# Performance work log

Measured on AMD Instinct MI355X. Metric: run time of the kernel, lower is better.

## Reference

```python
import jax, jax.numpy as jnp
import numpy as np

C = 512      # filters
G = 32       # groups
EPS = 1e-6

def setup_inputs() -> dict:
    key = jax.random.key(0)
    ks = jax.random.split(key, 10)
    B, H, W = 2, 64, 64
    inputs = jax.random.normal(ks[0], (B, H, W, C), dtype=jnp.float32)
    scale = 1.0 / np.sqrt(C)
    def w(k):
        return jax.random.normal(k, (C, C), dtype=jnp.float32) * scale
    return {
        "inputs": inputs,
        "gn_gamma": jnp.ones((C,), jnp.float32),
        "gn_beta": jnp.zeros((C,), jnp.float32),
        "wq": w(ks[1]), "bq": jnp.zeros((C,), jnp.float32),
        "wk": w(ks[2]), "bk": jnp.zeros((C,), jnp.float32),
        "wv": w(ks[3]), "bv": jnp.zeros((C,), jnp.float32),
        "wo": w(ks[4]), "bo": jnp.zeros((C,), jnp.float32),
    }

def _group_norm(x, gamma, beta):
    B, H, W, c = x.shape
    xg = x.reshape(B, H, W, G, c // G)
    mean = jnp.mean(xg, axis=(1, 2, 4), keepdims=True)
    var = jnp.var(xg, axis=(1, 2, 4), keepdims=True)
    xg = (xg - mean) * jax.lax.rsqrt(var + EPS)
    return xg.reshape(B, H, W, c) * gamma + beta

def reference(inputs, gn_gamma, gn_beta, wq, bq, wk, bk, wv, bv, wo, bo):
    B, H, W, c = inputs.shape
    x = _group_norm(inputs, gn_gamma, gn_beta)
    # 1x1 convs == per-pixel linear layers
    q = (x @ wq + bq).reshape(B, H * W, c)
    k = (x @ wk + bk).reshape(B, H * W, c)
    v = (x @ wv + bv).reshape(B, H * W, c)
    q = q * jnp.asarray(1.0 / np.sqrt(float(c)), q.dtype)
    scores = jnp.einsum('bnc,bmc->bnm', q, k).astype(jnp.float32)  # [B,N,N]
    probs = jax.nn.softmax(scores, axis=-1).astype(inputs.dtype)
    attn = jnp.einsum('bnm,bmc->bnc', probs, v)
    out = attn.reshape(B, H, W, c) @ wo + bo
    return out + inputs
```

## Files before the change

### kernel.cpp

```cpp
#include <hip/hip_runtime.h>
#include <math.h>

typedef __bf16 bf16;
typedef __bf16 bf16x8 __attribute__((ext_vector_type(8)));
typedef float  f32x4  __attribute__((ext_vector_type(4)));

#define DEV __device__ __forceinline__

DEV void gload_lds16(const bf16* g, bf16* l) {
  __builtin_amdgcn_global_load_lds(
      (const __attribute__((address_space(1))) void*)g,
      (__attribute__((address_space(3))) void*)l, 16, 0, 0);
}

#define OFF_STATS 0UL
#define OFF_XN    512UL
#define OFF_WTQKV 8389120UL
#define OFF_WOT   9961984UL
#define OFF_BIASQ 10486272UL
#define OFF_QKV   10492416UL
#define OFF_VT    35658240UL
#define OFF_S     44046848UL
#define OFF_ATTN  111155712UL

__global__ __launch_bounds__(256) void gn_part_k(const float* __restrict__ x,
                                                 float2* __restrict__ part) {
  const int blk = blockIdx.x;
  const int chunk = blk & 15;
  const int bg = blk >> 4;
  const int b = bg >> 5, g = bg & 31;
  const int t = threadIdx.x;
  const int p = chunk * 256 + t;
  const float* xp = x + (size_t)b * (4096 * 512) + (size_t)p * 512 + g * 16;
  float4 v0 = *(const float4*)(xp);
  float4 v1 = *(const float4*)(xp + 4);
  float4 v2 = *(const float4*)(xp + 8);
  float4 v3 = *(const float4*)(xp + 12);
  float s  = v0.x + v0.y + v0.z + v0.w + v1.x + v1.y + v1.z + v1.w
           + v2.x + v2.y + v2.z + v2.w + v3.x + v3.y + v3.z + v3.w;
  float ss = v0.x*v0.x + v0.y*v0.y + v0.z*v0.z + v0.w*v0.w
           + v1.x*v1.x + v1.y*v1.y + v1.z*v1.z + v1.w*v1.w
           + v2.x*v2.x + v2.y*v2.y + v2.z*v2.z + v2.w*v2.w
           + v3.x*v3.x + v3.y*v3.y + v3.z*v3.z + v3.w*v3.w;
#pragma unroll
  for (int off = 32; off; off >>= 1) {
    s  += __shfl_xor(s, off);
    ss += __shfl_xor(ss, off);
  }
  __shared__ float rs[4], rss[4];
  const int w = t >> 6, l = t & 63;
  if (l == 0) { rs[w] = s; rss[w] = ss; }
  __syncthreads();
  if (t == 0)
    part[blk] = make_float2(rs[0] + rs[1] + rs[2] + rs[3],
                            rss[0] + rss[1] + rss[2] + rss[3]);
}

__global__ void gn_finish_k(const float2* __restrict__ part,
                            float2* __restrict__ stats) {
  const int g = threadIdx.x;
  float s = 0.f, ss = 0.f;
#pragma unroll
  for (int c = 0; c < 16; ++c) {
    float2 p = part[g * 16 + c];
    s += p.x; ss += p.y;
  }
  float mean = s * (1.0f / 65536.0f);
  float var  = ss * (1.0f / 65536.0f) - mean * mean;
  stats[g] = make_float2(mean, 1.0f / sqrtf(var + 1e-6f));
}

__global__ __launch_bounds__(256) void gn_apply_k(const float* __restrict__ x,
                                                  const float2* __restrict__ stats,
                                                  const float* __restrict__ gamma,
                                                  const float* __restrict__ beta,
                                                  bf16* __restrict__ xn) {
  size_t i = ((size_t)blockIdx.x * 256 + threadIdx.x) * 8;
  const int c = (int)(i & 511);
  const int b = (int)(i >> 21);
  float2 st = stats[b * 32 + (c >> 4)];
  float4 xa = *(const float4*)(x + i);
  float4 xb = *(const float4*)(x + i + 4);
  float4 ga = *(const float4*)(gamma + c);
  float4 gb = *(const float4*)(gamma + c + 4);
  float4 ba = *(const float4*)(beta + c);
  float4 bb = *(const float4*)(beta + c + 4);
  bf16x8 o;
  o[0] = (bf16)((xa.x - st.x) * st.y * ga.x + ba.x);
  o[1] = (bf16)((xa.y - st.x) * st.y * ga.y + ba.y);
  o[2] = (bf16)((xa.z - st.x) * st.y * ga.z + ba.z);
  o[3] = (bf16)((xa.w - st.x) * st.y * ga.w + ba.w);
  o[4] = (bf16)((xb.x - st.x) * st.y * gb.x + bb.x);
  o[5] = (bf16)((xb.y - st.x) * st.y * gb.y + bb.y);
  o[6] = (bf16)((xb.z - st.x) * st.y * gb.z + bb.z);
  o[7] = (bf16)((xb.w - st.x) * st.y * gb.w + bb.w);
  *(bf16x8*)(xn + i) = o;
}

__global__ void prep_w_k(const float* __restrict__ wq, const float* __restrict__ wk,
                         const float* __restrict__ wv, const float* __restrict__ wo,
                         bf16* __restrict__ wt_qkv, bf16* __restrict__ wot, float qscale) {
  const int z = blockIdx.z;
  const float* W = (z == 0) ? wq : (z == 1) ? wk : (z == 2) ? wv : wo;
  bf16* dst = (z < 3) ? (wt_qkv + (size_t)z * 512 * 512) : wot;
  const float s = (z == 0) ? qscale : 1.0f;
  __shared__ float tile[32][33];
  const int i0 = blockIdx.y * 32;
  const int o0 = blockIdx.x * 32;
#pragma unroll
  for (int r = threadIdx.y; r < 32; r += 8)
    tile[r][threadIdx.x] = W[(size_t)(i0 + r) * 512 + o0 + threadIdx.x];
  __syncthreads();
#pragma unroll
  for (int r = threadIdx.y; r < 32; r += 8)
    dst[(size_t)(o0 + r) * 512 + i0 + threadIdx.x] = (bf16)(tile[threadIdx.x][r] * s);
}

__global__ void prep_bias_k(const float* __restrict__ bq, const float* __restrict__ bk,
                            const float* __restrict__ bv, float* __restrict__ bias_qkv,
                            float qscale) {
  int i = blockIdx.x * 256 + threadIdx.x;
  float v = (i < 512) ? bq[i] * qscale : (i < 1024) ? bk[i - 512] : bv[i - 1024];
  bias_qkv[i] = v;
}

__global__ void transpose_v_k(const bf16* __restrict__ qkv, bf16* __restrict__ vt) {
  __shared__ bf16 tile[32][33];
  const int z = blockIdx.z;
  const int n0 = blockIdx.x * 32, d0 = blockIdx.y * 32;
  const bf16* src = qkv + (size_t)z * 4096 * 1536 + 1024;
#pragma unroll
  for (int r = threadIdx.y; r < 32; r += 8)
    tile[r][threadIdx.x] = src[(size_t)(n0 + r) * 1536 + d0 + threadIdx.x];
  __syncthreads();
  bf16* dst = vt + (size_t)z * 512 * 4096;
#pragma unroll
  for (int r = threadIdx.y; r < 32; r += 8)
    dst[(size_t)(d0 + r) * 4096 + n0 + threadIdx.x] = tile[threadIdx.x][r];
}

__global__ __launch_bounds__(256) void softmax_k(bf16* __restrict__ S) {
  const int t = threadIdx.x;
  bf16* p = S + (size_t)blockIdx.x * 4096 + t * 16;
  bf16x8 u0 = *(const bf16x8*)p;
  bf16x8 u1 = *(const bf16x8*)(p + 8);
  float v[16];
#pragma unroll
  for (int j = 0; j < 8; ++j) { v[j] = (float)u0[j]; v[j + 8] = (float)u1[j]; }
  float m = v[0];
#pragma unroll
  for (int j = 1; j < 16; ++j) m = fmaxf(m, v[j]);
#pragma unroll
  for (int off = 32; off; off >>= 1) m = fmaxf(m, __shfl_xor(m, off));
  __shared__ float red[4];
  const int w = t >> 6, l = t & 63;
  if (l == 0) red[w] = m;
  __syncthreads();
  m = fmaxf(fmaxf(red[0], red[1]), fmaxf(red[2], red[3]));
  __syncthreads();
  float s = 0.f;
#pragma unroll
  for (int j = 0; j < 16; ++j) { v[j] = __expf(v[j] - m); s += v[j]; }
#pragma unroll
  for (int off = 32; off; off >>= 1) s += __shfl_xor(s, off);
  if (l == 0) red[w] = s;
  __syncthreads();
  s = red[0] + red[1] + red[2] + red[3];
  const float inv = 1.0f / s;
#pragma unroll
  for (int j = 0; j < 8; ++j) { u0[j] = (bf16)(v[j] * inv); u1[j] = (bf16)(v[j + 8] * inv); }
  *(bf16x8*)p = u0;
  *(bf16x8*)(p + 8) = u1;
}

template <int BM, int BN, int EPI, int GX, int GY, int GZ>
__global__ __launch_bounds__(256, 2) void gemm_nt(
    const bf16* __restrict__ A, int lda, long sAz,
    const bf16* __restrict__ B, int ldb, long sBz,
    void* __restrict__ C, int ldc, long sCz,
    int nk,
    const float* __restrict__ bias,
    const float* __restrict__ resid) {
  constexpr int WM = BM / 2, WN = BN / 2;
  constexpr int FM = BM / 32, FN = BN / 32;
  constexpr int NWG = GX * GY * GZ;
  constexpr int CPX = NWG / 8;
  __shared__ alignas(16) bf16 As[2][BM * 32];
  __shared__ alignas(16) bf16 Bs[2][BN * 32];

  const int lin = blockIdx.x;
  const int wid = (lin & 7) * CPX + (lin >> 3);
  const int bx = wid % GX;
  const int by = (wid / GX) % GY;
  const int bz = wid / (GX * GY);

  const int t = threadIdx.x;
  const bf16* Aq = A + (size_t)bz * sAz + (size_t)by * BM * lda;
  const bf16* Bq = B + (size_t)bz * sBz + (size_t)bx * BN * ldb;

  auto stage = [&](int buf, int kt) {
    const int k0 = kt * 32;
#pragma unroll
    for (int i = 0; i < BM / 64; ++i) {
      int r = i * 64 + (t >> 2);
      gload_lds16(Aq + (size_t)r * lda + k0 + (t & 3) * 8, &As[buf][i * 2048 + t * 8]);
    }
#pragma unroll
    for (int i = 0; i < BN / 64; ++i) {
      int r = i * 64 + (t >> 2);
      gload_lds16(Bq + (size_t)r * ldb + k0 + (t & 3) * 8, &Bs[buf][i * 2048 + t * 8]);
    }
  };

  const int l = t & 63, w = t >> 6;
  const int wr = w >> 1, wc = w & 1;
  const int lr = l & 15, kh = l >> 4;

  f32x4 acc[FM][FN] = {};

  stage(0, 0);
  for (int kt = 0; kt < nk; ++kt) {
    __syncthreads();
    if (kt + 1 < nk) stage((kt + 1) & 1, kt + 1);
    const int buf = kt & 1;
    const bf16* ap = &As[buf][(wr * WM + lr) * 32 + kh * 8];
    const bf16* bp = &Bs[buf][(wc * WN + lr) * 32 + kh * 8];
    bf16x8 a[FM], b[FN];
#pragma unroll
    for (int m = 0; m < FM; ++m) a[m] = *(const bf16x8*)(ap + m * 16 * 32);
#pragma unroll
    for (int n = 0; n < FN; ++n) b[n] = *(const bf16x8*)(bp + n * 16 * 32);
#pragma unroll
    for (int m = 0; m < FM; ++m)
#pragma unroll
      for (int n = 0; n < FN; ++n)
        acc[m][n] = __builtin_amdgcn_mfma_f32_16x16x32_bf16(a[m], b[n], acc[m][n], 0, 0, 0);
  }

  const int gr0 = by * BM + wr * WM + kh * 4;
  const int gc0 = bx * BN + wc * WN + lr;
#pragma unroll
  for (int m = 0; m < FM; ++m)
#pragma unroll
    for (int n = 0; n < FN; ++n) {
      const int c = gc0 + n * 16;
      float bv = 0.f;
      if constexpr (EPI >= 1) bv = bias[c];
#pragma unroll
      for (int j = 0; j < 4; ++j) {
        const int r = gr0 + m * 16 + j;
        float val = acc[m][n][j] + bv;
        if constexpr (EPI == 2) {
          float* Cf = (float*)C + (size_t)bz * sCz;
          Cf[(size_t)r * ldc + c] = val + resid[(size_t)r * ldc + c];
        } else {
          bf16* Cb = (bf16*)C + (size_t)bz * sCz;
          Cb[(size_t)r * ldc + c] = (bf16)val;
        }
      }
    }
}

extern "C" void kernel_launch(void* const* d_in, const int* in_sizes, int n_in,
                              void* d_out, int out_size, void* d_ws, size_t ws_size,
                              hipStream_t stream) {
  const float* x     = (const float*)d_in[0];
  const float* gamma = (const float*)d_in[1];
  const float* beta  = (const float*)d_in[2];
  const float* wq = (const float*)d_in[3];
  const float* bq = (const float*)d_in[4];
  const float* wk = (const float*)d_in[5];
  const float* bk = (const float*)d_in[6];
  const float* wv = (const float*)d_in[7];
  const float* bv = (const float*)d_in[8];
  const float* wo = (const float*)d_in[9];
  const float* bo = (const float*)d_in[10];
  float* out = (float*)d_out;
  char* ws = (char*)d_ws;

  float2* stats    = (float2*)(ws + OFF_STATS);
  bf16*   xn       = (bf16*)(ws + OFF_XN);
  bf16*   wt_qkv   = (bf16*)(ws + OFF_WTQKV);
  bf16*   wot      = (bf16*)(ws + OFF_WOT);
  float*  bias_qkv = (float*)(ws + OFF_BIASQ);
  bf16*   qkv      = (bf16*)(ws + OFF_QKV);
  bf16*   vt       = (bf16*)(ws + OFF_VT);
  bf16*   S        = (bf16*)(ws + OFF_S);
  bf16*   attn     = (bf16*)(ws + OFF_ATTN);
  float2* gn_part  = (float2*)(ws + OFF_S);

  const float qscale = 0.04419417382415922f;

  prep_w_k<<<dim3(16, 16, 4), dim3(32, 8), 0, stream>>>(wq, wk, wv, wo, wt_qkv, wot, qscale);
  prep_bias_k<<<6, 256, 0, stream>>>(bq, bk, bv, bias_qkv, qscale);
  gn_part_k<<<1024, 256, 0, stream>>>(x, gn_part);
  gn_finish_k<<<1, 64, 0, stream>>>(gn_part, stats);
  gn_apply_k<<<2048, 256, 0, stream>>>(x, stats, gamma, beta, xn);

  gemm_nt<128, 128, 1, 12, 64, 1><<<768, 256, 0, stream>>>(
      xn, 512, 0, wt_qkv, 512, 0, qkv, 1536, 0, 512 / 32, bias_qkv, nullptr);

  gemm_nt<128, 128, 0, 32, 32, 2><<<2048, 256, 0, stream>>>(
      qkv, 1536, 4096L * 1536, qkv + 512, 1536, 4096L * 1536,
      S, 4096, 4096L * 4096, 512 / 32, nullptr, nullptr);

  softmax_k<<<8192, 256, 0, stream>>>(S);

  transpose_v_k<<<dim3(128, 16, 2), dim3(32, 8), 0, stream>>>(qkv, vt);

  gemm_nt<128, 64, 0, 8, 32, 2><<<512, 256, 0, stream>>>(
      S, 4096, 4096L * 4096, vt, 4096, 512L * 4096,
      attn, 512, 4096L * 512, 4096 / 32, nullptr, nullptr);

  gemm_nt<64, 128, 2, 4, 128, 1><<<512, 256, 0, stream>>>(
      attn, 512, 0, wot, 512, 0, out, 512, 0, 512 / 32, bo, x);
}
```

Baseline: 200.9 us.

## Double K-tile depth to 64 and XOR-swizzle LDS layout in GEMM

The bf16 GEMM kernel now stages 64-wide K slices per iteration instead of 32, which halves the number of barrier/stage iterations. Each row's 16-byte chunks are XOR-swizzled by row index so that fragment reads from LDS avoid bank conflicts. This doubles the LDS footprint per block, which may reduce occupancy, and raises register use from holding two k-halves of fragments.

```diff
diff --git a/kernel.cpp b/kernel.cpp
--- a/kernel.cpp
+++ b/kernel.cpp
@@ -185,8 +185,8 @@
   constexpr int FM = BM / 32, FN = BN / 32;
   constexpr int NWG = GX * GY * GZ;
   constexpr int CPX = NWG / 8;
-  __shared__ alignas(16) bf16 As[2][BM * 32];
-  __shared__ alignas(16) bf16 Bs[2][BN * 32];
+  __shared__ alignas(16) bf16 As[2][BM * 64];
+  __shared__ alignas(16) bf16 Bs[2][BN * 64];
 
   const int lin = blockIdx.x;
   const int wid = (lin & 7) * CPX + (lin >> 3);
@@ -198,23 +198,23 @@
   const bf16* Aq = A + (size_t)bz * sAz + (size_t)by * BM * lda;
   const bf16* Bq = B + (size_t)bz * sBz + (size_t)bx * BN * ldb;
 
+  const int srow = t >> 3;
+  const int sg   = (t & 7) ^ (srow & 7);
+
   auto stage = [&](int buf, int kt) {
-    const int k0 = kt * 32;
-#pragma unroll
-    for (int i = 0; i < BM / 64; ++i) {
-      int r = i * 64 + (t >> 2);
-      gload_lds16(Aq + (size_t)r * lda + k0 + (t & 3) * 8, &As[buf][i * 2048 + t * 8]);
-    }
-#pragma unroll
-    for (int i = 0; i < BN / 64; ++i) {
-      int r = i * 64 + (t >> 2);
-      gload_lds16(Bq + (size_t)r * ldb + k0 + (t & 3) * 8, &Bs[buf][i * 2048 + t * 8]);
-    }
+    const int k0 = kt * 64 + sg * 8;
+#pragma unroll
+    for (int i = 0; i < BM / 32; ++i)
+      gload_lds16(Aq + (size_t)(i * 32 + srow) * lda + k0, &As[buf][i * 2048 + t * 8]);
+#pragma unroll
+    for (int i = 0; i < BN / 32; ++i)
+      gload_lds16(Bq + (size_t)(i * 32 + srow) * ldb + k0, &Bs[buf][i * 2048 + t * 8]);
   };
 
   const int l = t & 63, w = t >> 6;
   const int wr = w >> 1, wc = w & 1;
   const int lr = l & 15, kh = l >> 4;
+  const int rs = lr & 7;
 
   f32x4 acc[FM][FN] = {};
 
@@ -223,18 +223,24 @@
     __syncthreads();
     if (kt + 1 < nk) stage((kt + 1) & 1, kt + 1);
     const int buf = kt & 1;
-    const bf16* ap = &As[buf][(wr * WM + lr) * 32 + kh * 8];
-    const bf16* bp = &Bs[buf][(wc * WN + lr) * 32 + kh * 8];
-    bf16x8 a[FM], b[FN];
-#pragma unroll
-    for (int m = 0; m < FM; ++m) a[m] = *(const bf16x8*)(ap + m * 16 * 32);
-#pragma unroll
-    for (int n = 0; n < FN; ++n) b[n] = *(const bf16x8*)(bp + n * 16 * 32);
-#pragma unroll
-    for (int m = 0; m < FM; ++m)
+    bf16x8 a[2][FM], b[2][FN];
+#pragma unroll
+    for (int h = 0; h < 2; ++h) {
+      const int g = ((h * 4 + kh) ^ rs) * 8;
+#pragma unroll
+      for (int m = 0; m < FM; ++m)
+        a[h][m] = *(const bf16x8*)(&As[buf][(wr * WM + m * 16 + lr) * 64 + g]);
 #pragma unroll
       for (int n = 0; n < FN; ++n)
-        acc[m][n] = __builtin_amdgcn_mfma_f32_16x16x32_bf16(a[m], b[n], acc[m][n], 0, 0, 0);
+        b[h][n] = *(const bf16x8*)(&Bs[buf][(wc * WN + n * 16 + lr) * 64 + g]);
+    }
+#pragma unroll
+    for (int h = 0; h < 2; ++h)
+#pragma unroll
+      for (int m = 0; m < FM; ++m)
+#pragma unroll
+        for (int n = 0; n < FN; ++n)
+          acc[m][n] = __builtin_amdgcn_mfma_f32_16x16x32_bf16(a[h][m], b[h][n], acc[m][n], 0, 0, 0);
   }
 
   const int gr0 = by * BM + wr * WM + kh * 4;
@@ -298,11 +304,11 @@
   gn_apply_k<<<2048, 256, 0, stream>>>(x, stats, gamma, beta, xn);
 
   gemm_nt<128, 128, 1, 12, 64, 1><<<768, 256, 0, stream>>>(
-      xn, 512, 0, wt_qkv, 512, 0, qkv, 1536, 0, 512 / 32, bias_qkv, nullptr);
+      xn, 512, 0, wt_qkv, 512, 0, qkv, 1536, 0, 512 / 64, bias_qkv, nullptr);
 
   gemm_nt<128, 128, 0, 32, 32, 2><<<2048, 256, 0, stream>>>(
       qkv, 1536, 4096L * 1536, qkv + 512, 1536, 4096L * 1536,
-      S, 4096, 4096L * 4096, 512 / 32, nullptr, nullptr);
+      S, 4096, 4096L * 4096, 512 / 64, nullptr, nullptr);
 
   softmax_k<<<8192, 256, 0, stream>>>(S);
 
@@ -310,8 +316,8 @@
 
   gemm_nt<128, 64, 0, 8, 32, 2><<<512, 256, 0, stream>>>(
       S, 4096, 4096L * 4096, vt, 4096, 512L * 4096,
-      attn, 512, 4096L * 512, 4096 / 32, nullptr, nullptr);
+      attn, 512, 4096L * 512, 4096 / 64, nullptr, nullptr);
 
   gemm_nt<64, 128, 2, 4, 128, 1><<<512, 256, 0, stream>>>(
-      attn, 512, 0, wot, 512, 0, out, 512, 0, 512 / 32, bo, x);
-}
+      attn, 512, 0, wot, 512, 0, out, 512, 0, 512 / 64, bo, x);
+}
```

New measurement: 185.4 us. 1.08x faster.

## Replace double-buffered GEMM with 4-slot LDS ring, swizzle, and larger tiles

Applied to the files above, without the earlier changes.

Rewrites the bf16 GEMM kernel to keep a 4-deep LDS ring of K-slices. Explicit vmcnt waits and raw barriers replace the per-iteration __syncthreads, so three stages of global loads stay in flight while the MFMAs run. It also adds an XOR-style column rotation on the LDS layout to cut bank conflicts, raises wave priority around the MFMA block, and changes tile shapes per call (256x256 with 8 waves for QK^T, 128x128 for PV and the output projection). The risks are higher LDS use (256x256 tiles over 4 slots is 128KB), which may cut occupancy, and fewer workgroups on the smaller GEMMs.

```diff
diff --git a/kernel.cpp b/kernel.cpp
--- a/kernel.cpp
+++ b/kernel.cpp
@@ -6,6 +6,8 @@
 typedef float  f32x4  __attribute__((ext_vector_type(4)));
 
 #define DEV __device__ __forceinline__
+#define VMCNT(n) asm volatile("s_waitcnt vmcnt(" #n ")" ::: "memory")
+#define CFENCE  asm volatile("" ::: "memory")
 
 DEV void gload_lds16(const bf16* g, bf16* l) {
   __builtin_amdgcn_global_load_lds(
@@ -173,20 +175,22 @@
   *(bf16x8*)(p + 8) = u1;
 }
 
-template <int BM, int BN, int EPI, int GX, int GY, int GZ>
-__global__ __launch_bounds__(256, 2) void gemm_nt(
+template <int BM, int BN, int WR, int WC, int EPI, int GX, int GY, int GZ>
+__global__ __launch_bounds__(64 * WR * WC, 2) void gemm_ring(
     const bf16* __restrict__ A, int lda, long sAz,
     const bf16* __restrict__ B, int ldb, long sBz,
     void* __restrict__ C, int ldc, long sCz,
-    int nk,
+    int ns,
     const float* __restrict__ bias,
     const float* __restrict__ resid) {
-  constexpr int WM = BM / 2, WN = BN / 2;
-  constexpr int FM = BM / 32, FN = BN / 32;
+  constexpr int T = 64 * WR * WC;
+  constexpr int WM = BM / WR, WN = BN / WC;
+  constexpr int FM = WM / 16, FN = WN / 16;
   constexpr int NWG = GX * GY * GZ;
   constexpr int CPX = NWG / 8;
-  __shared__ alignas(16) bf16 As[2][BM * 32];
-  __shared__ alignas(16) bf16 Bs[2][BN * 32];
+  static_assert(BM * 32 == T * 16 && BN * 32 == T * 16, "2 loads per operand per slot");
+  __shared__ alignas(16) bf16 As[4][BM][32];
+  __shared__ alignas(16) bf16 Bs[4][BN][32];
 
   const int lin = blockIdx.x;
   const int wid = (lin & 7) * CPX + (lin >> 3);
@@ -198,43 +202,62 @@
   const bf16* Aq = A + (size_t)bz * sAz + (size_t)by * BM * lda;
   const bf16* Bq = B + (size_t)bz * sBz + (size_t)bx * BN * ldb;
 
-  auto stage = [&](int buf, int kt) {
-    const int k0 = kt * 32;
-#pragma unroll
-    for (int i = 0; i < BM / 64; ++i) {
-      int r = i * 64 + (t >> 2);
-      gload_lds16(Aq + (size_t)r * lda + k0 + (t & 3) * 8, &As[buf][i * 2048 + t * 8]);
+  auto stage = [&](int ss) {
+    const int r4 = ss & 3;
+    const int k0 = ss * 32;
+#pragma unroll
+    for (int j = 0; j < 2; ++j) {
+      const int row = j * (T / 4) + (t >> 2);
+      const int gs = ((t & 3) - (row >> 1)) & 3;
+      gload_lds16(Aq + (size_t)row * lda + k0 + gs * 8,
+                  &As[r4][0][0] + j * (T * 8) + t * 8);
     }
 #pragma unroll
-    for (int i = 0; i < BN / 64; ++i) {
-      int r = i * 64 + (t >> 2);
-      gload_lds16(Bq + (size_t)r * ldb + k0 + (t & 3) * 8, &Bs[buf][i * 2048 + t * 8]);
+    for (int j = 0; j < 2; ++j) {
+      const int row = j * (T / 4) + (t >> 2);
+      const int gs = ((t & 3) - (row >> 1)) & 3;
+      gload_lds16(Bq + (size_t)row * ldb + k0 + gs * 8,
+                  &Bs[r4][0][0] + j * (T * 8) + t * 8);
     }
   };
 
   const int l = t & 63, w = t >> 6;
-  const int wr = w >> 1, wc = w & 1;
+  const int wr = w / WC, wc = w % WC;
   const int lr = l & 15, kh = l >> 4;
+  const int gp = ((kh + (lr >> 1)) & 3) * 8;
 
   f32x4 acc[FM][FN] = {};
 
-  stage(0, 0);
-  for (int kt = 0; kt < nk; ++kt) {
-    __syncthreads();
-    if (kt + 1 < nk) stage((kt + 1) & 1, kt + 1);
-    const int buf = kt & 1;
-    const bf16* ap = &As[buf][(wr * WM + lr) * 32 + kh * 8];
-    const bf16* bp = &Bs[buf][(wc * WN + lr) * 32 + kh * 8];
+#pragma unroll
+  for (int p = 0; p < 3; ++p)
+    if (p < ns) stage(p);
+
+  for (int s = 0; s < ns; ++s) {
+    if (s + 3 < ns) stage(s + 3);
+    const int ahead = ns - 1 - s;
+    if (ahead >= 3)      VMCNT(12);
+    else if (ahead == 2) VMCNT(8);
+    else if (ahead == 1) VMCNT(4);
+    else                 VMCNT(0);
+    __builtin_amdgcn_s_barrier();
+    CFENCE;
+    const int r4 = s & 3;
+    const bf16* ap = &As[r4][wr * WM + lr][0] + gp;
+    const bf16* bp = &Bs[r4][wc * WN + lr][0] + gp;
     bf16x8 a[FM], b[FN];
 #pragma unroll
     for (int m = 0; m < FM; ++m) a[m] = *(const bf16x8*)(ap + m * 16 * 32);
 #pragma unroll
     for (int n = 0; n < FN; ++n) b[n] = *(const bf16x8*)(bp + n * 16 * 32);
+    __builtin_amdgcn_s_setprio(1);
 #pragma unroll
     for (int m = 0; m < FM; ++m)
 #pragma unroll
       for (int n = 0; n < FN; ++n)
         acc[m][n] = __builtin_amdgcn_mfma_f32_16x16x32_bf16(a[m], b[n], acc[m][n], 0, 0, 0);
+    __builtin_amdgcn_s_setprio(0);
+    CFENCE;
+    __builtin_amdgcn_s_barrier();
   }
 
   const int gr0 = by * BM + wr * WM + kh * 4;
@@ -297,21 +320,21 @@
   gn_finish_k<<<1, 64, 0, stream>>>(gn_part, stats);
   gn_apply_k<<<2048, 256, 0, stream>>>(x, stats, gamma, beta, xn);
 
-  gemm_nt<128, 128, 1, 12, 64, 1><<<768, 256, 0, stream>>>(
-      xn, 512, 0, wt_qkv, 512, 0, qkv, 1536, 0, 512 / 32, bias_qkv, nullptr);
-
-  gemm_nt<128, 128, 0, 32, 32, 2><<<2048, 256, 0, stream>>>(
+  gemm_ring<128, 128, 2, 2, 1, 12, 64, 1><<<768, 256, 0, stream>>>(
+      xn, 512, 0, wt_qkv, 512, 0, qkv, 1536, 0, 16, bias_qkv, nullptr);
+
+  gemm_ring<256, 256, 2, 4, 0, 16, 16, 2><<<512, 512, 0, stream>>>(
       qkv, 1536, 4096L * 1536, qkv + 512, 1536, 4096L * 1536,
-      S, 4096, 4096L * 4096, 512 / 32, nullptr, nullptr);
+      S, 4096, 4096L * 4096, 16, nullptr, nullptr);
 
   softmax_k<<<8192, 256, 0, stream>>>(S);
 
   transpose_v_k<<<dim3(128, 16, 2), dim3(32, 8), 0, stream>>>(qkv, vt);
 
-  gemm_nt<128, 64, 0, 8, 32, 2><<<512, 256, 0, stream>>>(
+  gemm_ring<128, 128, 2, 2, 0, 4, 32, 2><<<256, 256, 0, stream>>>(
       S, 4096, 4096L * 4096, vt, 4096, 512L * 4096,
-      attn, 512, 4096L * 512, 4096 / 32, nullptr, nullptr);
-
-  gemm_nt<64, 128, 2, 4, 128, 1><<<512, 256, 0, stream>>>(
-      attn, 512, 0, wot, 512, 0, out, 512, 0, 512 / 32, bo, x);
-}
+      attn, 512, 4096L * 512, 128, nullptr, nullptr);
+
+  gemm_ring<128, 128, 2, 2, 2, 4, 64, 1><<<256, 256, 0, stream>>>(
+      attn, 512, 0, wot, 512, 0, out, 512, 0, 16, bo, x);
+}
```

Result: slower. 215.8 us (+7.4%).
